# Optimization experiments

Measured on AMD Instinct MI355X. Metric: run time of the kernel, lower is better.

## Reference

```python
import jax, jax.numpy as jnp
import numpy as np

TS = 1.5          # hard-coded sampling period in forward()
W_CENTER = 337.927  # hard-coded center frequency in forward()


def shg_mat(yta):
    """Vectorized createSHGmat: yta is a complex64 vector of length N.
    Row m: Ts * fftshift(fft(fftshift(yta * roll(yta, delay[m]) * shiftFactor))).
    torch.roll(x, s)[j] == x[(j - s) % N], matching the gather below."""
    N = yta.shape[0]
    delays_f = jnp.arange(-(N // 2), N // 2, dtype=jnp.float32)
    delays_i = jnp.arange(-(N // 2), N // 2, dtype=jnp.int32)
    shift_factor = jnp.exp(-1j * 2.0 * W_CENTER * TS * delays_f).astype(jnp.complex64)  # [N]
    idx = (jnp.arange(N, dtype=jnp.int32)[None, :] - delays_i[:, None]) % N  # [N, N]
    y_shift = yta[idx]                                    # [N(delay), N(elem)]
    prod = yta[None, :] * y_shift * shift_factor[None, :]  # elementwise, [N, N]
    prod = jnp.fft.fftshift(prod, axes=-1)
    mat = TS * jnp.fft.fftshift(jnp.fft.fft(prod, axis=-1), axes=-1)
    return mat  # complex64 [N, N]


def frog_error(Tref, Tmeas):
    """calcFrogError: scalar FROG error between reference and measured traces."""
    mu = jnp.sum(Tmeas @ Tref) / jnp.sum(Tref @ Tref)
    r = jnp.sum((Tmeas - mu * Tref) ** 2)
    norm = jnp.float32(Tmeas.size) * jnp.max(Tmeas) ** 2
    return jnp.sqrt(r / norm)


def setup_inputs() -> dict:
    key = jax.random.key(0)
    k1, k2, k3 = jax.random.split(key, 3)
    B, N = 8, 1024
    prediction = jax.random.normal(k1, (B, 2 * N), dtype=jnp.float32)
    label = jax.random.normal(k2, (B, 2 * N), dtype=jnp.float32)
    spectrogram = jax.random.uniform(k3, (N, N), dtype=jnp.float32)
    return {"prediction": prediction, "label": label, "spectrogram": spectrogram}


def reference(prediction, label, spectrogram):
    B, two_n = prediction.shape
    n = two_n // 2
    pred_analytical = (prediction[:, :n] + 1j * prediction[:, n:]).astype(jnp.complex64)  # [B, N]
    mats = jax.vmap(shg_mat)(pred_analytical)          # [B, N, N] complex64
    Tref = jnp.abs(mats)                               # predicted SHG trace magnitude
    errs = jax.vmap(lambda t: frog_error(t, spectrogram))(Tref)  # [B]
    # loss = (sum over batch of frog_error) / batch_size; masked MSE terms in the
    # original are computed but never added to the returned loss, so they are omitted.
    return jnp.mean(errs)
```

## Files before the change

### kernel.cpp

```cpp
#include <hip/hip_runtime.h>
#include <math.h>

#define N 1024
#define B_ 8
#define T_ 256
#define R_ 8
#define NREP 4

#define OFF_SF      0
#define OFF_TW      2048
#define OFF_ROWSUM  10240
#define ZERO_START  18432
#define OFF_COLSUMM 18432
#define OFF_SUMM2   19456
#define OFF_MAXM    19457
#define OFF_SUMMT   19464
#define OFF_SUMTT   19472
#define OFF_COLT    20480
#define WS_END      (OFF_COLT + B_ * NREP * N)

#define S1(a) ((a) ^ (((a) >> 2) & 0x10))
#define S2(a) ((a) ^ (((a) >> 3) & 0x0C))
#define S3(a) ((a) ^ (((a) >> 5) & 0x07))
#define S4(a) ((a) ^ (((a) >> 5) & 0x07))

__device__ __forceinline__ float wave_sum(float v) {
    #pragma unroll
    for (int o = 32; o > 0; o >>= 1) v += __shfl_down(v, o, 64);
    return v;
}
__device__ __forceinline__ float wave_max(float v) {
    #pragma unroll
    for (int o = 32; o > 0; o >>= 1) v = fmaxf(v, __shfl_down(v, o, 64));
    return v;
}

__device__ __forceinline__ void load_tw(float tw[6], const float* __restrict__ p) {
    float4 v = *(const float4*)p;
    float2 w = *(const float2*)(p + 4);
    tw[0] = v.x; tw[1] = v.y; tw[2] = v.z; tw[3] = v.w; tw[4] = w.x; tw[5] = w.y;
}

__device__ __forceinline__ void bfly4(float xr[4], float xi[4], const float tw[6]) {
    float t0r = xr[0] + xr[2], t0i = xi[0] + xi[2];
    float t1r = xr[0] - xr[2], t1i = xi[0] - xi[2];
    float t2r = xr[1] + xr[3], t2i = xi[1] + xi[3];
    float t3r = xr[1] - xr[3], t3i = xi[1] - xi[3];
    float y1r = t1r + t3i, y1i = t1i - t3r;
    float y2r = t0r - t2r, y2i = t0i - t2i;
    float y3r = t1r - t3i, y3i = t1i + t3r;
    xr[0] = t0r + t2r;            xi[0] = t0i + t2i;
    xr[1] = y1r * tw[0] - y1i * tw[1]; xi[1] = y1r * tw[1] + y1i * tw[0];
    xr[2] = y2r * tw[2] - y2i * tw[3]; xi[2] = y2r * tw[3] + y2i * tw[2];
    xr[3] = y3r * tw[4] - y3i * tw[5]; xi[3] = y3r * tw[5] + y3i * tw[4];
}

__global__ __launch_bounds__(T_) void k_prep(float* ws) {
    const int e = blockIdx.x * T_ + threadIdx.x;
    {
        double ang = -2.0 * 337.927 * 1.5 * (double)(e - 512);
        double s, c;
        sincos(ang, &s, &c);
        ws[OFF_SF + 2 * e] = (float)c;
        ws[OFF_SF + 2 * e + 1] = (float)s;
    }
    {
        int s = e >> 8, tt = e & 255;
        int h = 256 >> (2 * s);
        int pos = tt & (h - 1);
        int step = 1 << (2 * s);
        double a1 = -2.0 * M_PI * (double)(pos * step) / 1024.0;
        double s1, c1, s2, c2, s3, c3;
        sincos(a1, &s1, &c1);
        sincos(2.0 * a1, &s2, &c2);
        sincos(3.0 * a1, &s3, &c3);
        float* p = ws + OFF_TW + e * 8;
        p[0] = (float)c1; p[1] = (float)s1;
        p[2] = (float)c2; p[3] = (float)s2;
        p[4] = (float)c3; p[5] = (float)s3;
        p[6] = 0.f; p[7] = 0.f;
    }
}

__global__ __launch_bounds__(T_) void k_mstats(const float* __restrict__ M, float* ws) {
    const int t = threadIdx.x;
    const int r0 = blockIdx.x * 16;
    float cs[4] = {0.f, 0.f, 0.f, 0.f};
    float sq = 0.f, mx = 0.f;
    for (int r = 0; r < 16; ++r) {
        const float* row = M + (size_t)(r0 + r) * N;
        #pragma unroll
        for (int q = 0; q < 4; ++q) {
            float v = row[t + T_ * q];
            cs[q] += v;
            sq += v * v;
            mx = fmaxf(mx, v);
        }
    }
    #pragma unroll
    for (int q = 0; q < 4; ++q) atomicAdd(&ws[OFF_COLSUMM + t + T_ * q], cs[q]);
    sq = wave_sum(sq);
    mx = wave_max(mx);
    __shared__ float rs_[4], rm_[4];
    int wid = t >> 6, lane = t & 63;
    if (lane == 0) { rs_[wid] = sq; rm_[wid] = mx; }
    __syncthreads();
    if (t == 0) {
        atomicAdd(&ws[OFF_SUMM2], rs_[0] + rs_[1] + rs_[2] + rs_[3]);
        float X = fmaxf(fmaxf(rm_[0], rm_[1]), fmaxf(rm_[2], rm_[3]));
        atomicMax((unsigned int*)ws + OFF_MAXM, __float_as_uint(X));
    }
}

__global__ __launch_bounds__(T_, 4) void k_row(const float* __restrict__ pred,
                                               const float* __restrict__ M,
                                               float* __restrict__ ws) {
    __shared__ float Yr[N], Yi[N];
    __shared__ float Ar[N], Ai[N], Br[N], Bi[N];
    __shared__ float colA[N];
    __shared__ float red[3][4];
    const int t = threadIdx.x;
    const int m0 = blockIdx.x * R_;
    const int b = blockIdx.y;
    const int wid = t >> 6, lane = t & 63;

    {
        const float* pr = pred + (size_t)b * 2 * N;
        #pragma unroll
        for (int q = 0; q < 4; ++q) {
            int j = t + T_ * q;
            Yr[j] = pr[j];
            Yi[j] = pr[N + j];
            colA[j] = 0.f;
        }
    }
    __syncthreads();

    float mtacc = 0.f, ttacc = 0.f;
    float xr[4], xi[4], tw[6];

    for (int r = 0; r < R_; ++r) {
        const int m = m0 + r;

        {
            const float2* sf2 = (const float2*)(ws + OFF_SF);
            #pragma unroll
            for (int q = 0; q < 4; ++q) {
                int j = t + T_ * q;
                int s = (j - m + 512) & (N - 1);
                float ar = Yr[j], ai = Yi[j];
                float br = Yr[s], bi = Yi[s];
                float2 sv = sf2[j];
                float p_r = ar * br - ai * bi;
                float p_i = ar * bi + ai * br;
                xr[q] = p_r * sv.x - p_i * sv.y;
                xi[q] = p_r * sv.y + p_i * sv.x;
            }
            load_tw(tw, ws + OFF_TW + (size_t)t * 8);
            bfly4(xr, xi, tw);
            #pragma unroll
            for (int q = 0; q < 4; ++q) { int a = t + 256 * q; Ar[a] = xr[q]; Ai[a] = xi[q]; }
        }
        __syncthreads();

        {
            int base = ((t >> 6) << 8) | (t & 63);
            #pragma unroll
            for (int q = 0; q < 4; ++q) { int a = base + (q << 6); xr[q] = Ar[a]; xi[q] = Ai[a]; }
            load_tw(tw, ws + OFF_TW + (size_t)(256 + t) * 8);
            bfly4(xr, xi, tw);
            #pragma unroll
            for (int q = 0; q < 4; ++q) { int a = S1(base + (q << 6)); Br[a] = xr[q]; Bi[a] = xi[q]; }
        }
        __syncthreads();

        {
            int base = ((t >> 4) << 6) | (t & 15);
            #pragma unroll
            for (int q = 0; q < 4; ++q) { int a = S1(base + (q << 4)); xr[q] = Br[a]; xi[q] = Bi[a]; }
            load_tw(tw, ws + OFF_TW + (size_t)(512 + t) * 8);
            bfly4(xr, xi, tw);
            #pragma unroll
            for (int q = 0; q < 4; ++q) { int a = S2(base + (q << 4)); Ar[a] = xr[q]; Ai[a] = xi[q]; }
        }
        __syncthreads();

        {
            int base = ((t >> 2) << 4) | (t & 3);
            #pragma unroll
            for (int q = 0; q < 4; ++q) { int a = S2(base + (q << 2)); xr[q] = Ar[a]; xi[q] = Ai[a]; }
            load_tw(tw, ws + OFF_TW + (size_t)(768 + t) * 8);
            bfly4(xr, xi, tw);
            #pragma unroll
            for (int q = 0; q < 4; ++q) { int a = S3(base + (q << 2)); Br[a] = xr[q]; Bi[a] = xi[q]; }
        }
        __syncthreads();

        {
            int base = t << 2;
            #pragma unroll
            for (int q = 0; q < 4; ++q) { int a = S3(base + q); xr[q] = Br[a]; xi[q] = Bi[a]; }
            float t0r = xr[0] + xr[2], t0i = xi[0] + xi[2];
            float t1r = xr[0] - xr[2], t1i = xi[0] - xi[2];
            float t2r = xr[1] + xr[3], t2i = xi[1] + xi[3];
            float t3r = xr[1] - xr[3], t3i = xi[1] - xi[3];
            float yr[4], yi[4];
            yr[0] = t0r + t2r; yi[0] = t0i + t2i;
            yr[1] = t1r + t3i; yi[1] = t1i - t3r;
            yr[2] = t0r - t2r; yi[2] = t0i - t2i;
            yr[3] = t1r - t3i; yi[3] = t1i + t3r;
            int r4t = ((t & 3) << 6) | (((t >> 2) & 3) << 4) | (((t >> 4) & 3) << 2) | ((t >> 6) & 3);
            #pragma unroll
            for (int q = 0; q < 4; ++q) {
                int c = ((q << 8) | r4t) ^ 512;
                Ar[S4(c)] = 1.5f * sqrtf(yr[q] * yr[q] + yi[q] * yi[q]);
            }
        }
        __syncthreads();

        {
            const float* Mrow = M + (size_t)m * N;
            float rs = 0.f;
            #pragma unroll
            for (int q = 0; q < 4; ++q) {
                int cc = t + 256 * q;
                float v = Ar[S4(cc)];
                rs += v;
                ttacc += v * v;
                mtacc += Mrow[cc] * v;
                colA[cc] += v;
            }
            rs = wave_sum(rs);
            if (lane == 0) red[0][wid] = rs;
            __syncthreads();
            if (t == 0) {
                ws[OFF_ROWSUM + b * N + m] = red[0][0] + red[0][1] + red[0][2] + red[0][3];
            }
        }
    }

    {
        float* colT = ws + OFF_COLT + (size_t)(b * NREP + (blockIdx.x & (NREP - 1))) * N;
        #pragma unroll
        for (int q = 0; q < 4; ++q) {
            int cc = t + 256 * q;
            atomicAdd(&colT[cc], colA[cc]);
        }
        float mt = wave_sum(mtacc);
        float tt2 = wave_sum(ttacc);
        if (lane == 0) { red[1][wid] = mt; red[2][wid] = tt2; }
        __syncthreads();
        if (t == 0) {
            atomicAdd(&ws[OFF_SUMMT + b], red[1][0] + red[1][1] + red[1][2] + red[1][3]);
            atomicAdd(&ws[OFF_SUMTT + b], red[2][0] + red[2][1] + red[2][2] + red[2][3]);
        }
    }
}

__global__ __launch_bounds__(T_) void k_final(float* ws, float* out) {
    __shared__ double redn[4], redd[4];
    const int b = blockIdx.x;
    const int t = threadIdx.x;
    const int wid = t >> 6, lane = t & 63;
    const float* rowsum = ws + OFF_ROWSUM + (size_t)b * N;
    double num = 0.0, den = 0.0;
    #pragma unroll
    for (int q = 0; q < 4; ++q) {
        int j = t + 256 * q;
        double r = (double)rowsum[j];
        float ct = 0.f;
        #pragma unroll
        for (int rep = 0; rep < NREP; ++rep)
            ct += ws[OFF_COLT + (size_t)(b * NREP + rep) * N + j];
        num += (double)ws[OFF_COLSUMM + j] * r;
        den += (double)ct * r;
    }
    #pragma unroll
    for (int o = 32; o > 0; o >>= 1) {
        num += __shfl_down(num, o, 64);
        den += __shfl_down(den, o, 64);
    }
    if (lane == 0) { redn[wid] = num; redd[wid] = den; }
    __syncthreads();
    if (t == 0) {
        double NUM = redn[0] + redn[1] + redn[2] + redn[3];
        double DEN = redd[0] + redd[1] + redd[2] + redd[3];
        double mu = NUM / DEN;
        double r = (double)ws[OFF_SUMM2] - 2.0 * mu * (double)ws[OFF_SUMMT + b]
                 + mu * mu * (double)ws[OFF_SUMTT + b];
        float mx = ws[OFF_MAXM];
        double norm = 1048576.0 * (double)mx * (double)mx;
        atomicAdd(out, (float)(sqrt(r / norm) / 8.0));
    }
}

extern "C" void kernel_launch(void* const* d_in, const int* in_sizes, int n_in,
                              void* d_out, int out_size, void* d_ws, size_t ws_size,
                              hipStream_t stream) {
    const float* pred = (const float*)d_in[0];
    const float* M = (const float*)d_in[2];
    float* ws = (float*)d_ws;
    float* out = (float*)d_out;

    hipMemsetAsync(ws + ZERO_START, 0, (size_t)(WS_END - ZERO_START) * sizeof(float), stream);
    hipMemsetAsync(out, 0, sizeof(float), stream);
    k_prep<<<4, T_, 0, stream>>>(ws);
    k_mstats<<<64, T_, 0, stream>>>(M, ws);
    dim3 grid(N / R_, B_);
    k_row<<<grid, T_, 0, stream>>>(pred, M, ws);
    k_final<<<B_, T_, 0, stream>>>(ws, out);
}
```

Measured before the change: 106.0 us.

## Restructure FFT as per-wave 1024-point transform, exploit row symmetry, fuse kernels

Replaces the block-wide radix-4 FFT, which needed __syncthreads between stages, with a per-wave FFT. Each wave holds 16 complex values per lane in registers and exchanges data through a private swizzled LDS buffer using only wave barriers. It uses the symmetry that row m and row N-m have equal magnitudes, so only about half the delay rows are transformed and results are weighted by two. The M-statistics kernel is folded into extra blocks of the row kernel, and the memsets move into the prep kernel, cutting launches. The risks are higher register pressure from 16-element arrays and a symmetry assumption that must hold exactly.

```diff
diff --git a/kernel.cpp b/kernel.cpp
--- a/kernel.cpp
+++ b/kernel.cpp
@@ -4,25 +4,21 @@
 #define N 1024
 #define B_ 8
 #define T_ 256
-#define R_ 8
 #define NREP 4
+#define NFFTBLK 1024
+#define NSTAT 64
 
 #define OFF_SF      0
-#define OFF_TW      2048
-#define OFF_ROWSUM  10240
-#define ZERO_START  18432
-#define OFF_COLSUMM 18432
-#define OFF_SUMM2   19456
-#define OFF_MAXM    19457
-#define OFF_SUMMT   19464
-#define OFF_SUMTT   19472
-#define OFF_COLT    20480
-#define WS_END      (OFF_COLT + B_ * NREP * N)
-
-#define S1(a) ((a) ^ (((a) >> 2) & 0x10))
-#define S2(a) ((a) ^ (((a) >> 3) & 0x0C))
-#define S3(a) ((a) ^ (((a) >> 5) & 0x07))
-#define S4(a) ((a) ^ (((a) >> 5) & 0x07))
+#define OFF_TA      2048
+#define OFF_ROWSUM  5120
+#define ZERO_START  13312
+#define OFF_COLSUMM 13312
+#define OFF_SUMM2   14336
+#define OFF_MAXM    14337
+#define OFF_SUMMT   14344
+#define OFF_SUMTT   14352
+#define OFF_COLT    14368
+#define ZERO_END    47136
 
 __device__ __forceinline__ float wave_sum(float v) {
     #pragma unroll
@@ -35,27 +31,40 @@
     return v;
 }
 
-__device__ __forceinline__ void load_tw(float tw[6], const float* __restrict__ p) {
-    float4 v = *(const float4*)p;
-    float2 w = *(const float2*)(p + 4);
-    tw[0] = v.x; tw[1] = v.y; tw[2] = v.z; tw[3] = v.w; tw[4] = w.x; tw[5] = w.y;
-}
-
-__device__ __forceinline__ void bfly4(float xr[4], float xi[4], const float tw[6]) {
-    float t0r = xr[0] + xr[2], t0i = xi[0] + xi[2];
-    float t1r = xr[0] - xr[2], t1i = xi[0] - xi[2];
-    float t2r = xr[1] + xr[3], t2i = xi[1] + xi[3];
-    float t3r = xr[1] - xr[3], t3i = xi[1] - xi[3];
-    float y1r = t1r + t3i, y1i = t1i - t3r;
-    float y2r = t0r - t2r, y2i = t0i - t2i;
-    float y3r = t1r - t3i, y3i = t1i + t3r;
-    xr[0] = t0r + t2r;            xi[0] = t0i + t2i;
-    xr[1] = y1r * tw[0] - y1i * tw[1]; xi[1] = y1r * tw[1] + y1i * tw[0];
-    xr[2] = y2r * tw[2] - y2i * tw[3]; xi[2] = y2r * tw[3] + y2i * tw[2];
-    xr[3] = y3r * tw[4] - y3i * tw[5]; xi[3] = y3r * tw[5] + y3i * tw[4];
-}
-
-__global__ __launch_bounds__(T_) void k_prep(float* ws) {
+#define BFLY4(x0, x1, x2, x3, w1, w2, w3)                                   \
+    do {                                                                    \
+        float t0r = x0.x + x2.x, t0i = x0.y + x2.y;                         \
+        float t1r = x0.x - x2.x, t1i = x0.y - x2.y;                         \
+        float t2r = x1.x + x3.x, t2i = x1.y + x3.y;                         \
+        float t3r = x1.x - x3.x, t3i = x1.y - x3.y;                         \
+        float y1r = t1r + t3i, y1i = t1i - t3r;                             \
+        float y2r = t0r - t2r, y2i = t0i - t2i;                             \
+        float y3r = t1r - t3i, y3i = t1i + t3r;                             \
+        x0 = make_float2(t0r + t2r, t0i + t2i);                             \
+        x1 = make_float2(y1r * w1.x - y1i * w1.y, y1r * w1.y + y1i * w1.x); \
+        x2 = make_float2(y2r * w2.x - y2i * w2.y, y2r * w2.y + y2i * w2.x); \
+        x3 = make_float2(y3r * w3.x - y3i * w3.y, y3r * w3.y + y3i * w3.x); \
+    } while (0)
+
+#define BFLY4_NOTW(x0, x1, x2, x3)                                          \
+    do {                                                                    \
+        float t0r = x0.x + x2.x, t0i = x0.y + x2.y;                         \
+        float t1r = x0.x - x2.x, t1i = x0.y - x2.y;                         \
+        float t2r = x1.x + x3.x, t2i = x1.y + x3.y;                         \
+        float t3r = x1.x - x3.x, t3i = x1.y - x3.y;                         \
+        x0 = make_float2(t0r + t2r, t0i + t2i);                             \
+        x1 = make_float2(t1r + t3i, t1i - t3r);                             \
+        x2 = make_float2(t0r - t2r, t0i - t2i);                             \
+        x3 = make_float2(t1r - t3i, t1i + t3r);                             \
+    } while (0)
+
+#define WSYNC()                                  \
+    do {                                         \
+        __builtin_amdgcn_s_waitcnt(0xc07f);      \
+        __builtin_amdgcn_wave_barrier();         \
+    } while (0)
+
+__global__ __launch_bounds__(T_) void k_prep(float* ws, float* out) {
     const int e = blockIdx.x * T_ + threadIdx.x;
     {
         double ang = -2.0 * 337.927 * 1.5 * (double)(e - 512);
@@ -64,195 +73,203 @@
         ws[OFF_SF + 2 * e] = (float)c;
         ws[OFF_SF + 2 * e + 1] = (float)s;
     }
-    {
-        int s = e >> 8, tt = e & 255;
-        int h = 256 >> (2 * s);
-        int pos = tt & (h - 1);
-        int step = 1 << (2 * s);
-        double a1 = -2.0 * M_PI * (double)(pos * step) / 1024.0;
+    if (e < 256) {
+        double a1 = -2.0 * M_PI * (double)e / 1024.0;
         double s1, c1, s2, c2, s3, c3;
         sincos(a1, &s1, &c1);
         sincos(2.0 * a1, &s2, &c2);
         sincos(3.0 * a1, &s3, &c3);
-        float* p = ws + OFF_TW + e * 8;
+        float* p = ws + OFF_TA + e * 6;
         p[0] = (float)c1; p[1] = (float)s1;
         p[2] = (float)c2; p[3] = (float)s2;
         p[4] = (float)c3; p[5] = (float)s3;
-        p[6] = 0.f; p[7] = 0.f;
-    }
-}
-
-__global__ __launch_bounds__(T_) void k_mstats(const float* __restrict__ M, float* ws) {
-    const int t = threadIdx.x;
-    const int r0 = blockIdx.x * 16;
-    float cs[4] = {0.f, 0.f, 0.f, 0.f};
-    float sq = 0.f, mx = 0.f;
-    for (int r = 0; r < 16; ++r) {
-        const float* row = M + (size_t)(r0 + r) * N;
-        #pragma unroll
-        for (int q = 0; q < 4; ++q) {
-            float v = row[t + T_ * q];
-            cs[q] += v;
-            sq += v * v;
-            mx = fmaxf(mx, v);
-        }
-    }
-    #pragma unroll
-    for (int q = 0; q < 4; ++q) atomicAdd(&ws[OFF_COLSUMM + t + T_ * q], cs[q]);
-    sq = wave_sum(sq);
-    mx = wave_max(mx);
-    __shared__ float rs_[4], rm_[4];
-    int wid = t >> 6, lane = t & 63;
-    if (lane == 0) { rs_[wid] = sq; rm_[wid] = mx; }
-    __syncthreads();
-    if (t == 0) {
-        atomicAdd(&ws[OFF_SUMM2], rs_[0] + rs_[1] + rs_[2] + rs_[3]);
-        float X = fmaxf(fmaxf(rm_[0], rm_[1]), fmaxf(rm_[2], rm_[3]));
-        atomicMax((unsigned int*)ws + OFF_MAXM, __float_as_uint(X));
-    }
+    }
+    for (int j = ZERO_START + e; j < ZERO_END; j += 4 * T_) ws[j] = 0.f;
+    if (e == 0) out[0] = 0.f;
 }
 
 __global__ __launch_bounds__(T_, 4) void k_row(const float* __restrict__ pred,
                                                const float* __restrict__ M,
                                                float* __restrict__ ws) {
-    __shared__ float Yr[N], Yi[N];
-    __shared__ float Ar[N], Ai[N], Br[N], Bi[N];
-    __shared__ float colA[N];
-    __shared__ float red[3][4];
-    const int t = threadIdx.x;
-    const int m0 = blockIdx.x * R_;
-    const int b = blockIdx.y;
-    const int wid = t >> 6, lane = t & 63;
+    __shared__ float2 Y[N];
+    __shared__ float2 XB[4][N];
+    const int tid = threadIdx.x;
+    const int lane = tid & 63;
+    const int wv = tid >> 6;
+    const int L = blockIdx.x;
+
+    if (L >= NFFTBLK) {
+        float* sred = (float*)&Y[0];
+        const int r0 = (L - NFFTBLK) * 16;
+        float cs[4] = {0.f, 0.f, 0.f, 0.f};
+        float sq = 0.f, mx = 0.f;
+        for (int r = 0; r < 16; ++r) {
+            const float* row = M + (size_t)(r0 + r) * N;
+            #pragma unroll
+            for (int q = 0; q < 4; ++q) {
+                float v = row[tid + T_ * q];
+                cs[q] += v;
+                sq += v * v;
+                mx = fmaxf(mx, v);
+            }
+        }
+        #pragma unroll
+        for (int q = 0; q < 4; ++q) atomicAdd(&ws[OFF_COLSUMM + tid + T_ * q], cs[q]);
+        sq = wave_sum(sq);
+        mx = wave_max(mx);
+        if (lane == 0) { sred[wv] = sq; sred[4 + wv] = mx; }
+        __syncthreads();
+        if (tid == 0) {
+            atomicAdd(&ws[OFF_SUMM2], sred[0] + sred[1] + sred[2] + sred[3]);
+            float X = fmaxf(fmaxf(sred[4], sred[5]), fmaxf(sred[6], sred[7]));
+            atomicMax((unsigned int*)ws + OFF_MAXM, __float_as_uint(X));
+        }
+        return;
+    }
+
+    const int b = L >> 7;
+    const int mgroup = L & 127;
 
     {
         const float* pr = pred + (size_t)b * 2 * N;
         #pragma unroll
         for (int q = 0; q < 4; ++q) {
-            int j = t + T_ * q;
-            Yr[j] = pr[j];
-            Yi[j] = pr[N + j];
-            colA[j] = 0.f;
-        }
-    }
-    __syncthreads();
-
+            int j = tid + T_ * q;
+            Y[j] = make_float2(pr[j], pr[N + j]);
+        }
+    }
+    __syncthreads();
+
+    const float2* sfg = (const float2*)(ws + OFF_SF);
+    const float2* TA  = (const float2*)(ws + OFF_TA);
+    float2* Xw = XB[wv];
+    const int g = lane & 15, a = lane >> 4;
+    const int c0 = ((lane & 3) << 4) | (((lane >> 2) & 3) << 2) | (lane >> 4);
+
+    float cr[16];
+    #pragma unroll
+    for (int i = 0; i < 16; ++i) cr[i] = 0.f;
     float mtacc = 0.f, ttacc = 0.f;
-    float xr[4], xi[4], tw[6];
-
-    for (int r = 0; r < R_; ++r) {
-        const int m = m0 + r;
-
+
+    const int nrow = (mgroup == 0 && wv == 0) ? 2 : 1;
+    for (int rr = 0; rr < nrow; ++rr) {
+        const int m = (rr == 0) ? (4 * mgroup + wv) : 512;
+        const int mm = (N - m) & (N - 1);
+        const float wgt = (mm == m) ? 1.f : 2.f;
+
+        float2 x[16];
+        #pragma unroll
+        for (int u = 0; u < 16; ++u) {
+            int j = lane + 64 * u;
+            int s = (j - m + 512) & (N - 1);
+            float2 ya = Y[j], yb = Y[s], sv = sfg[j];
+            float prr = ya.x * yb.x - ya.y * yb.y;
+            float pii = ya.x * yb.y + ya.y * yb.x;
+            x[u] = make_float2(prr * sv.x - pii * sv.y, prr * sv.y + pii * sv.x);
+        }
+        #pragma unroll
+        for (int k = 0; k < 4; ++k) {
+            int p3 = 3 * (lane + 64 * k);
+            float2 w1 = TA[p3], w2 = TA[p3 + 1], w3 = TA[p3 + 2];
+            BFLY4(x[k], x[k + 4], x[k + 8], x[k + 12], w1, w2, w3);
+        }
         {
-            const float2* sf2 = (const float2*)(ws + OFF_SF);
+            int p3 = 3 * (4 * lane);
+            float2 w1 = TA[p3], w2 = TA[p3 + 1], w3 = TA[p3 + 2];
             #pragma unroll
-            for (int q = 0; q < 4; ++q) {
-                int j = t + T_ * q;
-                int s = (j - m + 512) & (N - 1);
-                float ar = Yr[j], ai = Yi[j];
-                float br = Yr[s], bi = Yi[s];
-                float2 sv = sf2[j];
-                float p_r = ar * br - ai * bi;
-                float p_i = ar * bi + ai * br;
-                xr[q] = p_r * sv.x - p_i * sv.y;
-                xi[q] = p_r * sv.y + p_i * sv.x;
-            }
-            load_tw(tw, ws + OFF_TW + (size_t)t * 8);
-            bfly4(xr, xi, tw);
+            for (int k = 0; k < 4; ++k)
+                BFLY4(x[4 * k], x[4 * k + 1], x[4 * k + 2], x[4 * k + 3], w1, w2, w3);
+        }
+        #pragma unroll
+        for (int u = 0; u < 16; ++u) Xw[64 * u + (lane ^ u)] = x[u];
+        WSYNC();
+        float2 v[16];
+        #pragma unroll
+        for (int l = 0; l < 4; ++l) {
             #pragma unroll
-            for (int q = 0; q < 4; ++q) { int a = t + 256 * q; Ar[a] = xr[q]; Ai[a] = xi[q]; }
-        }
-        __syncthreads();
-
+            for (int j = 0; j < 4; ++j)
+                v[4 * l + j] = Xw[64 * g + 16 * j + ((4 * a + l) ^ g)];
+        }
+        #pragma unroll
+        for (int l = 0; l < 4; ++l) {
+            int p3 = 3 * (16 * (4 * a + l));
+            float2 w1 = TA[p3], w2 = TA[p3 + 1], w3 = TA[p3 + 2];
+            BFLY4(v[4 * l], v[4 * l + 1], v[4 * l + 2], v[4 * l + 3], w1, w2, w3);
+        }
+        WSYNC();
+        #pragma unroll
+        for (int l = 0; l < 4; ++l) {
+            #pragma unroll
+            for (int j = 0; j < 4; ++j)
+                Xw[64 * g + 16 * j + ((4 * a + l) ^ (4 * (g & 3) + j) ^ (g >> 2))] = v[4 * l + j];
+        }
+        WSYNC();
+        float2 z[16];
+        #pragma unroll
+        for (int r = 0; r < 16; ++r)
+            z[r] = Xw[16 * lane + (r ^ (lane & 15) ^ (lane >> 4))];
         {
-            int base = ((t >> 6) << 8) | (t & 63);
-            #pragma unroll
-            for (int q = 0; q < 4; ++q) { int a = base + (q << 6); xr[q] = Ar[a]; xi[q] = Ai[a]; }
-            load_tw(tw, ws + OFF_TW + (size_t)(256 + t) * 8);
-            bfly4(xr, xi, tw);
-            #pragma unroll
-            for (int q = 0; q < 4; ++q) { int a = S1(base + (q << 6)); Br[a] = xr[q]; Bi[a] = xi[q]; }
-        }
-        __syncthreads();
-
-        {
-            int base = ((t >> 4) << 6) | (t & 15);
-            #pragma unroll
-            for (int q = 0; q < 4; ++q) { int a = S1(base + (q << 4)); xr[q] = Br[a]; xi[q] = Bi[a]; }
-            load_tw(tw, ws + OFF_TW + (size_t)(512 + t) * 8);
-            bfly4(xr, xi, tw);
-            #pragma unroll
-            for (int q = 0; q < 4; ++q) { int a = S2(base + (q << 4)); Ar[a] = xr[q]; Ai[a] = xi[q]; }
-        }
-        __syncthreads();
-
-        {
-            int base = ((t >> 2) << 4) | (t & 3);
-            #pragma unroll
-            for (int q = 0; q < 4; ++q) { int a = S2(base + (q << 2)); xr[q] = Ar[a]; xi[q] = Ai[a]; }
-            load_tw(tw, ws + OFF_TW + (size_t)(768 + t) * 8);
-            bfly4(xr, xi, tw);
-            #pragma unroll
-            for (int q = 0; q < 4; ++q) { int a = S3(base + (q << 2)); Br[a] = xr[q]; Bi[a] = xi[q]; }
-        }
-        __syncthreads();
-
-        {
-            int base = t << 2;
-            #pragma unroll
-            for (int q = 0; q < 4; ++q) { int a = S3(base + q); xr[q] = Br[a]; xi[q] = Bi[a]; }
-            float t0r = xr[0] + xr[2], t0i = xi[0] + xi[2];
-            float t1r = xr[0] - xr[2], t1i = xi[0] - xi[2];
-            float t2r = xr[1] + xr[3], t2i = xi[1] + xi[3];
-            float t3r = xr[1] - xr[3], t3i = xi[1] - xi[3];
-            float yr[4], yi[4];
-            yr[0] = t0r + t2r; yi[0] = t0i + t2i;
-            yr[1] = t1r + t3i; yi[1] = t1i - t3r;
-            yr[2] = t0r - t2r; yi[2] = t0i - t2i;
-            yr[3] = t1r - t3i; yi[3] = t1i + t3r;
-            int r4t = ((t & 3) << 6) | (((t >> 2) & 3) << 4) | (((t >> 4) & 3) << 2) | ((t >> 6) & 3);
-            #pragma unroll
-            for (int q = 0; q < 4; ++q) {
-                int c = ((q << 8) | r4t) ^ 512;
-                Ar[S4(c)] = 1.5f * sqrtf(yr[q] * yr[q] + yi[q] * yi[q]);
-            }
-        }
-        __syncthreads();
-
-        {
-            const float* Mrow = M + (size_t)m * N;
-            float rs = 0.f;
-            #pragma unroll
-            for (int q = 0; q < 4; ++q) {
-                int cc = t + 256 * q;
-                float v = Ar[S4(cc)];
-                rs += v;
-                ttacc += v * v;
-                mtacc += Mrow[cc] * v;
-                colA[cc] += v;
-            }
-            rs = wave_sum(rs);
-            if (lane == 0) red[0][wid] = rs;
-            __syncthreads();
-            if (t == 0) {
-                ws[OFF_ROWSUM + b * N + m] = red[0][0] + red[0][1] + red[0][2] + red[0][3];
-            }
-        }
-    }
-
+            const float2 C1a = {0.92387953f, -0.38268343f}, C1b = {0.70710678f, -0.70710678f},
+                         C1c = {0.38268343f, -0.92387953f};
+            const float2 C2a = {0.70710678f, -0.70710678f}, C2b = {0.0f, -1.0f},
+                         C2c = {-0.70710678f, -0.70710678f};
+            const float2 C3a = {0.38268343f, -0.92387953f}, C3b = {-0.70710678f, -0.70710678f},
+                         C3c = {-0.92387953f, 0.38268343f};
+            BFLY4_NOTW(z[0], z[4], z[8], z[12]);
+            BFLY4(z[1], z[5], z[9], z[13], C1a, C1b, C1c);
+            BFLY4(z[2], z[6], z[10], z[14], C2a, C2b, C2c);
+            BFLY4(z[3], z[7], z[11], z[15], C3a, C3b, C3c);
+        }
+        #pragma unroll
+        for (int r4 = 0; r4 < 4; ++r4)
+            BFLY4_NOTW(z[4 * r4], z[4 * r4 + 1], z[4 * r4 + 2], z[4 * r4 + 3]);
+
+        float rs = 0.f;
+        const float* M1 = M + (size_t)m * N;
+        const float* M2 = M + (size_t)mm * N;
+        #pragma unroll
+        for (int r = 0; r < 16; ++r) {
+            float mag = 1.5f * sqrtf(z[r].x * z[r].x + z[r].y * z[r].y);
+            int c = 256 * ((r & 3) ^ 2) + 64 * (r >> 2) + c0;
+            rs += mag;
+            ttacc += wgt * mag * mag;
+            float ms = M1[c];
+            if (mm != m) ms += M2[c];
+            mtacc += ms * mag;
+            cr[r] += wgt * mag;
+        }
+        rs = wave_sum(rs);
+        if (lane == 0) {
+            ws[OFF_ROWSUM + b * N + m] = rs;
+            if (mm != m) ws[OFF_ROWSUM + b * N + mm] = rs;
+        }
+        WSYNC();
+    }
+
+    mtacc = wave_sum(mtacc);
+    ttacc = wave_sum(ttacc);
+    if (lane == 0) {
+        atomicAdd(&ws[OFF_SUMMT + b], mtacc);
+        atomicAdd(&ws[OFF_SUMTT + b], ttacc);
+    }
+
+    __syncthreads();
+    float* colM = (float*)&XB[0][0];
+    #pragma unroll
+    for (int q = 0; q < 4; ++q) colM[tid + T_ * q] = 0.f;
+    __syncthreads();
+    #pragma unroll
+    for (int r = 0; r < 16; ++r) {
+        int c = 256 * ((r & 3) ^ 2) + 64 * (r >> 2) + c0;
+        atomicAdd(&colM[c], cr[r]);
+    }
+    __syncthreads();
     {
-        float* colT = ws + OFF_COLT + (size_t)(b * NREP + (blockIdx.x & (NREP - 1))) * N;
+        float* colT = ws + OFF_COLT + (size_t)(b * NREP + (mgroup & (NREP - 1))) * N;
         #pragma unroll
         for (int q = 0; q < 4; ++q) {
-            int cc = t + 256 * q;
-            atomicAdd(&colT[cc], colA[cc]);
-        }
-        float mt = wave_sum(mtacc);
-        float tt2 = wave_sum(ttacc);
-        if (lane == 0) { red[1][wid] = mt; red[2][wid] = tt2; }
-        __syncthreads();
-        if (t == 0) {
-            atomicAdd(&ws[OFF_SUMMT + b], red[1][0] + red[1][1] + red[1][2] + red[1][3]);
-            atomicAdd(&ws[OFF_SUMTT + b], red[2][0] + red[2][1] + red[2][2] + red[2][3]);
+            int c = tid + T_ * q;
+            atomicAdd(&colT[c], colM[c]);
         }
     }
 }
@@ -302,11 +319,7 @@
     float* ws = (float*)d_ws;
     float* out = (float*)d_out;
 
-    hipMemsetAsync(ws + ZERO_START, 0, (size_t)(WS_END - ZERO_START) * sizeof(float), stream);
-    hipMemsetAsync(out, 0, sizeof(float), stream);
-    k_prep<<<4, T_, 0, stream>>>(ws);
-    k_mstats<<<64, T_, 0, stream>>>(M, ws);
-    dim3 grid(N / R_, B_);
-    k_row<<<grid, T_, 0, stream>>>(pred, M, ws);
+    k_prep<<<4, T_, 0, stream>>>(ws, out);
+    k_row<<<NFFTBLK + NSTAT, T_, 0, stream>>>(pred, M, ws);
     k_final<<<B_, T_, 0, stream>>>(ws, out);
 }
```

Result: slower. 155.1 us (+46.3%).
